# Optimization experiments

Hardware: AMD Instinct MI355X
Metric: run time of the kernel (lower is better)

Reference implementation:

```python
import jax, jax.numpy as jnp
import numpy as np

ETYPES = ((0, 2), (4, 6))  # per-metapath edge-type indices into the doubled r_vec table
ALPHA = 3.0


def celu3(x):
    return jax.nn.celu(x, alpha=ALPHA)


def cmul(a, b):
    # complex multiply, last dim = (real, imag)
    re = a[..., 0] * b[..., 0] - a[..., 1] * b[..., 1]
    im = a[..., 0] * b[..., 1] + a[..., 1] * b[..., 0]
    return jnp.stack([re, im], axis=-1)


def setup_inputs() -> dict:
    key = jax.random.key(0)
    ks = jax.random.split(key, 10)
    N, H, heads, M, E, P = 50000, 64, 4, 2, 250000, 3
    R, FH = 4, 128
    D = heads * H
    return {
        "features": jax.random.normal(ks[0], (N, H), jnp.float32),
        "r_vec": jax.random.normal(ks[1], (R, H // 2, 2), jnp.float32),
        "attn1_w": jax.random.normal(ks[2], (heads, H), jnp.float32) * 0.1,
        "attn2": jax.random.normal(ks[3], (1, heads, H), jnp.float32) * 0.1,
        "fw1": jax.random.normal(ks[4], (2 * FH, D), jnp.float32) * 0.05,
        "fb1": jnp.zeros((2 * FH,), jnp.float32),
        "fw2": jax.random.normal(ks[5], (FH, 2 * FH), jnp.float32) * 0.05,
        "fb2": jnp.zeros((FH,), jnp.float32),
        "fw3": jax.random.normal(ks[6], (1, FH), jnp.float32) * 0.05,
        "instances": jax.random.randint(ks[7], (M, E, P), 0, N, jnp.int32),
    }


def reference(features, r_vec, attn1_w, attn2, fw1, fb1, fw2, fb2, fw3, instances):
    N, H = features.shape
    M, E, P = instances.shape
    heads = attn1_w.shape[0]
    # unit-modulus rotations + conjugates: [2R, H/2, 2], even=r, odd=conj(r)
    rv = r_vec / jnp.linalg.norm(r_vec, axis=2, keepdims=True)
    conj = rv * jnp.array([1.0, -1.0], rv.dtype)
    rv2 = jnp.stack([rv, conj], axis=1).reshape(-1, H // 2, 2)

    per_path = []
    for m in range(M):
        inst = instances[m]  # [E, P]
        # backward cumulative rotation: final_r[i] = prod_{j>=i} r_{etype[j]}, final_r[P-1]=1
        ident = jnp.stack([jnp.ones(H // 2, rv.dtype), jnp.zeros(H // 2, rv.dtype)], axis=-1)
        frs = [ident]
        for i in range(P - 2, -1, -1):
            frs.insert(0, cmul(frs[0], rv2[ETYPES[m][i]]))
        fr = jnp.stack(frs)  # [P, H/2, 2]
        # gather features along metapath and rotate (last position rotated by identity)
        edata = features[inst].reshape(E, P, H // 2, 2)
        rot = cmul(edata, fr[None])
        me = jnp.mean(rot.reshape(E, P, H), axis=1)  # [E, H]
        se = celu3(me) * jax.nn.sigmoid(me)  # gated metapath embedding
        eft = celu3(se)  # same across heads in original (tiled)
        seg = inst[:, 0]  # target node per instance
        a1 = celu3(features[seg] @ attn1_w.T)  # [E, heads]
        a2 = jnp.einsum('eh,kh->ek', eft, attn2[0])  # [E, heads]
        a = celu3(a1 + a2)
        # segment softmax over each node's instance set
        amax = jax.ops.segment_max(a, seg, num_segments=N)
        ex = jnp.exp(a - amax[seg])
        den = jax.ops.segment_sum(ex, seg, num_segments=N)
        attn = ex / den[seg]  # [E, heads]
        hsum = jax.ops.segment_sum(attn[:, :, None] * eft[:, None, :], seg, num_segments=N)
        per_path.append(celu3(hsum).reshape(N, heads * H))  # empty nodes -> 0

    z = jnp.stack(per_path, axis=1)  # [N, M, D]
    t = celu3(z @ fw1.T + fb1)
    t = celu3(t @ fw2.T + fb2)
    w = (t @ fw3.T).mean(axis=0)  # [M, 1]
    beta = jax.nn.softmax(w, axis=0)
    out = (beta * z).sum(axis=1)  # [N, D]
    return out
```

## Files before the change

kernel.cpp:

```cpp
#include <hip/hip_runtime.h>
#include <hip/hip_bf16.h>

typedef unsigned short u16;
typedef unsigned int   u32;
typedef short bf16x8 __attribute__((ext_vector_type(8)));
typedef float f32x4  __attribute__((ext_vector_type(4)));

#define CAP 64

__device__ inline float b2f(u16 u){ return __builtin_bit_cast(float, (u32)u << 16); }
__device__ inline u16 f2b(float f){
  u32 x = __builtin_bit_cast(u32, f);
  x += 0x7fffu + ((x >> 16) & 1u);
  return (u16)(x >> 16);
}
__device__ inline u32 pk2(float lo, float hi){
  float2 f; f.x = lo; f.y = hi;
  __hip_bfloat162 h = __float22bfloat162_rn(f);
  u32 r; __builtin_memcpy(&r, &h, 4);
  return r;
}
__device__ inline void up2(u32 u, float& lo, float& hi){
  lo = __builtin_bit_cast(float, u << 16);
  hi = __builtin_bit_cast(float, u & 0xffff0000u);
}
__device__ inline float fexp(float x){ return __expf(x); }
__device__ inline float celu3(float x){
  return x > 0.f ? x : 3.f * (__expf(x * (1.f/3.f)) - 1.f);
}
__device__ inline float sigm(float x){ return 1.f / (1.f + __expf(-x)); }

__global__ __launch_bounds__(256) void conv_kernel(
    const float* __restrict__ src, u16* __restrict__ dst, int n8)
{
  int i = blockIdx.x * 256 + threadIdx.x;
  if (i >= n8) return;
  float4 a = ((const float4*)src)[2*i], b = ((const float4*)src)[2*i + 1];
  uint4 o;
  o.x = pk2(a.x, a.y);
  o.y = pk2(a.z, a.w);
  o.z = pk2(b.x, b.y);
  o.w = pk2(b.z, b.w);
  ((uint4*)dst)[i] = o;
}

__global__ __launch_bounds__(256) void a1_kernel(
    const float* __restrict__ feat, const float* __restrict__ attn1,
    u16* __restrict__ featb, float* __restrict__ a1c, int N)
{
  __shared__ float w1s[256];
  int t = threadIdx.x;
  w1s[t] = attn1[t];
  __syncthreads();
  int g = t >> 4, l = t & 15;
  int n = blockIdx.x * 16 + g;
  if (n >= N) return;
  float4 x = ((const float4*)feat)[(size_t)n*16 + l];
  uint2 o;
  o.x = pk2(x.x, x.y);
  o.y = pk2(x.z, x.w);
  ((uint2*)featb)[(size_t)n*16 + l] = o;
  float d[4];
  #pragma unroll
  for (int k = 0; k < 4; ++k){
    int wb = k*64 + l*4;
    d[k] = x.x*w1s[wb] + x.y*w1s[wb+1] + x.z*w1s[wb+2] + x.w*w1s[wb+3];
  }
  #pragma unroll
  for (int off = 8; off; off >>= 1){
    #pragma unroll
    for (int k = 0; k < 4; ++k) d[k] += __shfl_xor(d[k], off);
  }
  if (l == 0){
    float4 av;
    av.x = celu3(d[0]); av.y = celu3(d[1]);
    av.z = celu3(d[2]); av.w = celu3(d[3]);
    ((float4*)a1c)[n] = av;
  }
}

__global__ void fr_kernel(const float* __restrict__ rvec, float* __restrict__ fr){
  int c = threadIdx.x;
  if (c >= 32) return;
  for (int m = 0; m < 2; ++m){
    float ar = rvec[(2*m)*64 + c*2],   ai = rvec[(2*m)*64 + c*2 + 1];
    float br = rvec[(2*m+1)*64 + c*2], bi = rvec[(2*m+1)*64 + c*2 + 1];
    float na = rsqrtf(ar*ar + ai*ai); ar *= na; ai *= na;
    float nb = rsqrtf(br*br + bi*bi); br *= nb; bi *= nb;
    float* f = fr + m*128;
    f[c*2]        = br*ar - bi*ai;
    f[c*2 + 1]    = br*ai + bi*ar;
    f[64 + c*2]   = br;
    f[64 + c*2+1] = bi;
  }
}

__global__ __launch_bounds__(256) void edge_kernel(
    const u16* __restrict__ featb, const int* __restrict__ inst,
    const float* __restrict__ fr, const float* __restrict__ a1c,
    const float* __restrict__ attn2, u16* __restrict__ eft,
    float* __restrict__ a_ws, int* __restrict__ cnt, int* __restrict__ bucket,
    int E, int N)
{
  __shared__ float frs[128];
  __shared__ float w2s[256];
  int m = blockIdx.y;
  int t = threadIdx.x;
  if (t < 128) frs[t] = fr[m*128 + t];
  w2s[t] = attn2[t];
  __syncthreads();

  int g = t >> 4, l = t & 15;
  int e = blockIdx.x * 16 + g;
  if (e >= E) return;
  int base = (m*E + e)*3;
  int i0 = inst[base], i1 = inst[base+1], i2 = inst[base+2];

  const uint2* fb = (const uint2*)featb;
  uint2 v0 = fb[(size_t)i0*16 + l];
  uint2 v1 = fb[(size_t)i1*16 + l];
  uint2 v2 = fb[(size_t)i2*16 + l];
  float f0[4], f1[4], f2v[4];
  up2(v0.x, f0[0], f0[1]); up2(v0.y, f0[2], f0[3]);
  up2(v1.x, f1[0], f1[1]); up2(v1.y, f1[2], f1[3]);
  up2(v2.x, f2v[0], f2v[1]); up2(v2.y, f2v[2], f2v[3]);

  float4 R0 = *(const float4*)&frs[4*l];
  float4 R1 = *(const float4*)&frs[64 + 4*l];

  float mre0 = (f0[0]*R0.x - f0[1]*R0.y + f1[0]*R1.x - f1[1]*R1.y + f2v[0]) * (1.f/3.f);
  float mim0 = (f0[0]*R0.y + f0[1]*R0.x + f1[0]*R1.y + f1[1]*R1.x + f2v[1]) * (1.f/3.f);
  float mre1 = (f0[2]*R0.z - f0[3]*R0.w + f1[2]*R1.z - f1[3]*R1.w + f2v[2]) * (1.f/3.f);
  float mim1 = (f0[2]*R0.w + f0[3]*R0.z + f1[2]*R1.w + f1[3]*R1.z + f2v[3]) * (1.f/3.f);

  float ef[4], s;
  s = celu3(mre0) * sigm(mre0); ef[0] = celu3(s);
  s = celu3(mim0) * sigm(mim0); ef[1] = celu3(s);
  s = celu3(mre1) * sigm(mre1); ef[2] = celu3(s);
  s = celu3(mim1) * sigm(mim1); ef[3] = celu3(s);

  uint2 uo;
  uo.x = pk2(ef[0], ef[1]);
  uo.y = pk2(ef[2], ef[3]);
  ((uint2*)eft)[(size_t)(m*E + e)*16 + l] = uo;

  float d2[4];
  #pragma unroll
  for (int k = 0; k < 4; ++k){
    int wb = k*64 + l*4;
    d2[k] = ef[0]*w2s[wb] + ef[1]*w2s[wb+1] + ef[2]*w2s[wb+2] + ef[3]*w2s[wb+3];
  }
  #pragma unroll
  for (int off = 8; off; off >>= 1){
    #pragma unroll
    for (int k = 0; k < 4; ++k) d2[k] += __shfl_xor(d2[k], off);
  }
  if (l == 0){
    float4 a1v = ((const float4*)a1c)[i0];
    float4 av;
    av.x = celu3(a1v.x + d2[0]);
    av.y = celu3(a1v.y + d2[1]);
    av.z = celu3(a1v.z + d2[2]);
    av.w = celu3(a1v.w + d2[3]);
    ((float4*)a_ws)[m*E + e] = av;
    int pos = atomicAdd(&cnt[m*N + i0], 1);
    if (pos < CAP) bucket[(size_t)(m*N + i0)*CAP + pos] = e;
  }
}

__global__ __launch_bounds__(256) void seg_kernel(
    const float* __restrict__ a_ws, const u16* __restrict__ eft,
    const int* __restrict__ cnt, const int* __restrict__ bucket,
    u16* __restrict__ z, int E, int N)
{
  int m = blockIdx.y;
  int n = blockIdx.x * 4 + (threadIdx.x >> 6);
  if (n >= N) return;
  int lane = threadIdx.x & 63;
  int sidx = m*N + n;
  int deg = cnt[sidx]; if (deg > CAP) deg = CAP;

  float h0=0.f, h1=0.f, h2=0.f, h3=0.f;
  float d0=0.f, d1=0.f, d2=0.f, d3=0.f;
  if (deg > 0){
    const int* bk = bucket + (size_t)sidx * CAP;
    size_t ebase = (size_t)m * E;

    int e = (lane < deg) ? bk[lane] : 0;
    float w0 = 0.f, w1 = 0.f, w2 = 0.f, w3 = 0.f;
    if (lane < deg){
      float4 av = ((const float4*)a_ws)[ebase + e];
      w0 = fexp(av.x); w1 = fexp(av.y); w2 = fexp(av.z); w3 = fexp(av.w);
    }

    const u16* ep = eft + ebase*64;
    for (int j = 0; j < deg; ++j){
      int   ej  = __shfl(e,  j);
      float a0j = __shfl(w0, j), a1j = __shfl(w1, j);
      float a2j = __shfl(w2, j), a3j = __shfl(w3, j);
      float ev = b2f(ep[(size_t)ej*64 + lane]);
      h0 += a0j*ev; h1 += a1j*ev; h2 += a2j*ev; h3 += a3j*ev;
      d0 += a0j;    d1 += a1j;    d2 += a2j;    d3 += a3j;
    }
    h0 /= d0; h1 /= d1; h2 /= d2; h3 /= d3;
  }
  u16* zr = z + (size_t)sidx*256 + lane;
  zr[0]   = f2b(celu3(h0));
  zr[64]  = f2b(celu3(h1));
  zr[128] = f2b(celu3(h2));
  zr[192] = f2b(celu3(h3));
}

__global__ __launch_bounds__(256, 6) void mlp_kernel(
    const u16* __restrict__ z, const u16* __restrict__ fw1b, const float* __restrict__ fb1,
    const u16* __restrict__ fw2b, const float* __restrict__ fb2, const float* __restrict__ fw3,
    float* __restrict__ waccP, int rows, int N)
{
  __shared__ u16 buf[32][264];
  __shared__ float fw3s[128];
  __shared__ float sPart[4][32];
  int tid = threadIdx.x;
  int row0 = blockIdx.x * 32;

  if (tid < 128) fw3s[tid] = fw3[tid];

  const uint4* zg = (const uint4*)z;
  #pragma unroll
  for (int it = 0; it < 4; ++it){
    int idx = it*256 + tid;
    int row = idx >> 5;
    int c8  = idx & 31;
    uint4 v = make_uint4(0u,0u,0u,0u);
    int gr = row0 + row;
    if (gr < rows) v = zg[(size_t)gr*32 + c8];
    *(uint4*)&buf[row][c8*8] = v;
  }
  __syncthreads();

  int wv = tid >> 6, lane = tid & 63, lr = lane & 15, quad = lane >> 4;
  f32x4 zero4 = {0.f, 0.f, 0.f, 0.f};

  f32x4 acc[2][4];
  #pragma unroll
  for (int a = 0; a < 2; ++a)
    #pragma unroll
    for (int b = 0; b < 4; ++b) acc[a][b] = zero4;

  const u16* wb1 = fw1b + (size_t)(wv*64 + lr)*256 + quad*8;
  #pragma unroll
  for (int ks = 0; ks < 8; ++ks){
    bf16x8 bfr[4];
    #pragma unroll
    for (int nt = 0; nt < 4; ++nt)
      bfr[nt] = *(const bf16x8*)(wb1 + nt*16*256 + ks*32);
    #pragma unroll
    for (int mt = 0; mt < 2; ++mt){
      bf16x8 af = *(const bf16x8*)&buf[mt*16 + lr][ks*32 + quad*8];
      #pragma unroll
      for (int nt = 0; nt < 4; ++nt)
        acc[mt][nt] = __builtin_amdgcn_mfma_f32_16x16x32_bf16(af, bfr[nt], acc[mt][nt], 0, 0, 0);
    }
  }
  __syncthreads();
  #pragma unroll
  for (int nt = 0; nt < 4; ++nt){
    int col = wv*64 + nt*16 + lr;
    float bias = fb1[col];
    #pragma unroll
    for (int mt = 0; mt < 2; ++mt)
      #pragma unroll
      for (int ri = 0; ri < 4; ++ri){
        int row = mt*16 + quad*4 + ri;
        buf[row][col] = f2b(celu3(acc[mt][nt][ri] + bias));
      }
  }
  __syncthreads();

  f32x4 acc2[2][2];
  #pragma unroll
  for (int a = 0; a < 2; ++a){ acc2[a][0] = zero4; acc2[a][1] = zero4; }
  const u16* wb2 = fw2b + (size_t)(wv*32 + lr)*256 + quad*8;
  #pragma unroll
  for (int ks = 0; ks < 8; ++ks){
    bf16x8 cfr[2];
    cfr[0] = *(const bf16x8*)(wb2 + ks*32);
    cfr[1] = *(const bf16x8*)(wb2 + 16*256 + ks*32);
    #pragma unroll
    for (int mt = 0; mt < 2; ++mt){
      bf16x8 af = *(const bf16x8*)&buf[mt*16 + lr][ks*32 + quad*8];
      acc2[mt][0] = __builtin_amdgcn_mfma_f32_16x16x32_bf16(af, cfr[0], acc2[mt][0], 0, 0, 0);
      acc2[mt][1] = __builtin_amdgcn_mfma_f32_16x16x32_bf16(af, cfr[1], acc2[mt][1], 0, 0, 0);
    }
  }

  float ps[2][4];
  #pragma unroll
  for (int mt = 0; mt < 2; ++mt)
    #pragma unroll
    for (int ri = 0; ri < 4; ++ri) ps[mt][ri] = 0.f;
  #pragma unroll
  for (int nt = 0; nt < 2; ++nt){
    int col = wv*32 + nt*16 + lr;
    float bias = fb2[col];
    float w3 = fw3s[col];
    #pragma unroll
    for (int mt = 0; mt < 2; ++mt)
      #pragma unroll
      for (int ri = 0; ri < 4; ++ri)
        ps[mt][ri] += celu3(acc2[mt][nt][ri] + bias) * w3;
  }
  #pragma unroll
  for (int off = 8; off; off >>= 1)
    #pragma unroll
    for (int mt = 0; mt < 2; ++mt)
      #pragma unroll
      for (int ri = 0; ri < 4; ++ri)
        ps[mt][ri] += __shfl_xor(ps[mt][ri], off);
  if (lr == 0){
    #pragma unroll
    for (int mt = 0; mt < 2; ++mt)
      #pragma unroll
      for (int ri = 0; ri < 4; ++ri)
        sPart[wv][mt*16 + quad*4 + ri] = ps[mt][ri];
  }
  __syncthreads();

  if (tid < 32){
    float s = sPart[0][tid] + sPart[1][tid] + sPart[2][tid] + sPart[3][tid];
    int gr = row0 + tid;
    if (gr >= rows) s = 0.f;
    float s0 = (gr < N) ? s : 0.f;
    float s1 = (gr < N) ? 0.f : s;
    #pragma unroll
    for (int off = 16; off; off >>= 1){
      s0 += __shfl_xor(s0, off);
      s1 += __shfl_xor(s1, off);
    }
    if (tid == 0){
      int slot = blockIdx.x & 63;
      atomicAdd(&waccP[slot],      s0);
      atomicAdd(&waccP[64 + slot], s1);
    }
  }
}

__global__ void beta_kernel(float* __restrict__ wacc, float invN){
  int t = threadIdx.x;
  float s0 = wacc[t], s1 = wacc[64 + t];
  #pragma unroll
  for (int off = 32; off; off >>= 1){
    s0 += __shfl_xor(s0, off);
    s1 += __shfl_xor(s1, off);
  }
  if (t == 0){
    float w0 = s0*invN, w1 = s1*invN;
    float mx = fmaxf(w0, w1);
    float e0 = __expf(w0 - mx), e1 = __expf(w1 - mx);
    float s = e0 + e1;
    wacc[128] = e0 / s;
    wacc[129] = e1 / s;
  }
}

__global__ __launch_bounds__(256) void out_kernel(
    const u16* __restrict__ z, const float* __restrict__ wacc,
    float* __restrict__ out, int total)
{
  int idx = blockIdx.x * 256 + threadIdx.x;
  if (idx*8 >= total) return;
  float b0 = wacc[128], b1 = wacc[129];
  uint4 u0 = ((const uint4*)z)[idx];
  uint4 u1 = ((const uint4*)z)[(total >> 3) + idx];
  float a0,a1v,c0,c1;
  float4 o;
  up2(u0.x, a0, a1v); up2(u1.x, c0, c1);
  o.x = b0*a0 + b1*c0; o.y = b0*a1v + b1*c1;
  up2(u0.y, a0, a1v); up2(u1.y, c0, c1);
  o.z = b0*a0 + b1*c0; o.w = b0*a1v + b1*c1;
  ((float4*)out)[idx*2] = o;
  up2(u0.z, a0, a1v); up2(u1.z, c0, c1);
  o.x = b0*a0 + b1*c0; o.y = b0*a1v + b1*c1;
  up2(u0.w, a0, a1v); up2(u1.w, c0, c1);
  o.z = b0*a0 + b1*c0; o.w = b0*a1v + b1*c1;
  ((float4*)out)[idx*2 + 1] = o;
}

extern "C" void kernel_launch(void* const* d_in, const int* in_sizes, int n_in,
                              void* d_out, int out_size, void* d_ws, size_t ws_size,
                              hipStream_t stream)
{
  (void)n_in; (void)out_size; (void)ws_size;
  const float* feat  = (const float*)d_in[0];
  const float* rvec  = (const float*)d_in[1];
  const float* attn1 = (const float*)d_in[2];
  const float* attn2 = (const float*)d_in[3];
  const float* fw1   = (const float*)d_in[4];
  const float* fb1   = (const float*)d_in[5];
  const float* fw2   = (const float*)d_in[6];
  const float* fb2   = (const float*)d_in[7];
  const float* fw3   = (const float*)d_in[8];
  const int*   inst  = (const int*)d_in[9];

  int N = in_sizes[0] / 64;
  int E = in_sizes[9] / 6;

  char* ws = (char*)d_ws;
  u16*   z      = (u16*)ws;                            size_t zB = (size_t)2*N*256*2;
  u16*   eft    = (u16*)(ws + zB);                     size_t eB = (size_t)2*E*64*2;
  float* a_ws   = (float*)(ws + zB + eB);              size_t aB = (size_t)2*E*4*4;
  int*   bucket = (int*)(ws + zB + eB + aB);           size_t bB = (size_t)2*N*CAP*4;
  int*   cnt    = (int*)(ws + zB + eB + aB + bB);      size_t cB = (size_t)2*N*4;
  u16*   featb  = (u16*)(ws + zB + eB + aB + bB + cB); size_t fB = (size_t)N*64*2;
  float* a1c    = (float*)(ws + zB + eB + aB + bB + cB + fB);  size_t a1B = (size_t)N*4*4;
  u16*   fw1b   = (u16*)(ws + zB + eB + aB + bB + cB + fB + a1B);
  u16*   fw2b   = fw1b + 256*256;
  float* fr     = (float*)(fw2b + 128*256);
  float* wacc   = fr + 256;

  hipMemsetAsync(cnt, 0, cB, stream);
  hipMemsetAsync(wacc, 0, 128*sizeof(float), stream);

  a1_kernel<<<(N + 15)/16, 256, 0, stream>>>(feat, attn1, featb, a1c, N);
  conv_kernel<<<(256*256/8 + 255)/256, 256, 0, stream>>>(fw1, fw1b, 256*256/8);
  conv_kernel<<<(128*256/8 + 255)/256, 256, 0, stream>>>(fw2, fw2b, 128*256/8);
  fr_kernel<<<1, 64, 0, stream>>>(rvec, fr);
  edge_kernel<<<dim3((E + 15)/16, 2), 256, 0, stream>>>(
      featb, inst, fr, a1c, attn2, eft, a_ws, cnt, bucket, E, N);
  seg_kernel<<<dim3((N + 3)/4, 2), 256, 0, stream>>>(a_ws, eft, cnt, bucket, z, E, N);
  mlp_kernel<<<(2*N + 31)/32, 256, 0, stream>>>(z, fw1b, fb1, fw2b, fb2, fw3, wacc, 2*N, N);
  beta_kernel<<<1, 64, 0, stream>>>(wacc, 1.f/(float)N);
  out_kernel<<<((N*256/8) + 255)/256, 256, 0, stream>>>(z, wacc, (float*)d_out, N*256);
}
```

Before: 310.2 us.

## Retile MLP kernel to 64 rows, 8 waves with register-resident weight fragments

The MLP kernel now processes 64 rows per block with 512 threads (8 waves), each wave owning a narrower column slice (32 cols in layer 1, 16 in layer 2). All weight fragments for the wave are preloaded into registers up front, and the z tile load is issued to registers before the LDS store, so global loads overlap. This halves per-row weight traffic and moves layer-2 weight loads ahead of the barrier. The cost is higher register pressure and fewer, larger blocks.

```diff
diff --git a/kernel.cpp b/kernel.cpp
--- a/kernel.cpp
+++ b/kernel.cpp
@@ -211,63 +211,75 @@
   zr[192] = f2b(celu3(h3));
 }
 
-__global__ __launch_bounds__(256, 6) void mlp_kernel(
+__global__ __launch_bounds__(512, 4) void mlp_kernel(
     const u16* __restrict__ z, const u16* __restrict__ fw1b, const float* __restrict__ fb1,
     const u16* __restrict__ fw2b, const float* __restrict__ fb2, const float* __restrict__ fw3,
     float* __restrict__ waccP, int rows, int N)
 {
-  __shared__ u16 buf[32][264];
+  __shared__ u16 buf[64][264];
   __shared__ float fw3s[128];
-  __shared__ float sPart[4][32];
+  __shared__ float sPart[8][64];
   int tid = threadIdx.x;
-  int row0 = blockIdx.x * 32;
+  int row0 = blockIdx.x * 64;
+  int wv = tid >> 6, lane = tid & 63, lr = lane & 15, quad = lane >> 4;
+
+  const uint4* zg = (const uint4*)z;
+  uint4 zr4[4];
+  #pragma unroll
+  for (int it = 0; it < 4; ++it){
+    int idx = it*512 + tid;
+    int row = idx >> 5, c8 = idx & 31;
+    int gr = row0 + row;
+    zr4[it] = make_uint4(0u,0u,0u,0u);
+    if (gr < rows) zr4[it] = zg[(size_t)gr*32 + c8];
+  }
+
+  const u16* wb1 = fw1b + (size_t)(wv*32 + lr)*256 + quad*8;
+  bf16x8 B1[2][8];
+  #pragma unroll
+  for (int nt = 0; nt < 2; ++nt)
+    #pragma unroll
+    for (int ks = 0; ks < 8; ++ks)
+      B1[nt][ks] = *(const bf16x8*)(wb1 + nt*16*256 + ks*32);
 
   if (tid < 128) fw3s[tid] = fw3[tid];
 
-  const uint4* zg = (const uint4*)z;
   #pragma unroll
   for (int it = 0; it < 4; ++it){
-    int idx = it*256 + tid;
-    int row = idx >> 5;
-    int c8  = idx & 31;
-    uint4 v = make_uint4(0u,0u,0u,0u);
-    int gr = row0 + row;
-    if (gr < rows) v = zg[(size_t)gr*32 + c8];
-    *(uint4*)&buf[row][c8*8] = v;
-  }
-  __syncthreads();
-
-  int wv = tid >> 6, lane = tid & 63, lr = lane & 15, quad = lane >> 4;
+    int idx = it*512 + tid;
+    int row = idx >> 5, c8 = idx & 31;
+    *(uint4*)&buf[row][c8*8] = zr4[it];
+  }
+  __syncthreads();
+
   f32x4 zero4 = {0.f, 0.f, 0.f, 0.f};
 
-  f32x4 acc[2][4];
-  #pragma unroll
-  for (int a = 0; a < 2; ++a)
-    #pragma unroll
-    for (int b = 0; b < 4; ++b) acc[a][b] = zero4;
-
-  const u16* wb1 = fw1b + (size_t)(wv*64 + lr)*256 + quad*8;
+  f32x4 acc[4][2];
+  #pragma unroll
+  for (int a = 0; a < 4; ++a){ acc[a][0] = zero4; acc[a][1] = zero4; }
   #pragma unroll
   for (int ks = 0; ks < 8; ++ks){
-    bf16x8 bfr[4];
-    #pragma unroll
-    for (int nt = 0; nt < 4; ++nt)
-      bfr[nt] = *(const bf16x8*)(wb1 + nt*16*256 + ks*32);
-    #pragma unroll
-    for (int mt = 0; mt < 2; ++mt){
+    #pragma unroll
+    for (int mt = 0; mt < 4; ++mt){
       bf16x8 af = *(const bf16x8*)&buf[mt*16 + lr][ks*32 + quad*8];
-      #pragma unroll
-      for (int nt = 0; nt < 4; ++nt)
-        acc[mt][nt] = __builtin_amdgcn_mfma_f32_16x16x32_bf16(af, bfr[nt], acc[mt][nt], 0, 0, 0);
-    }
-  }
-  __syncthreads();
-  #pragma unroll
-  for (int nt = 0; nt < 4; ++nt){
-    int col = wv*64 + nt*16 + lr;
+      acc[mt][0] = __builtin_amdgcn_mfma_f32_16x16x32_bf16(af, B1[0][ks], acc[mt][0], 0, 0, 0);
+      acc[mt][1] = __builtin_amdgcn_mfma_f32_16x16x32_bf16(af, B1[1][ks], acc[mt][1], 0, 0, 0);
+    }
+  }
+
+  const u16* wb2 = fw2b + (size_t)(wv*16 + lr)*256 + quad*8;
+  bf16x8 B2[8];
+  #pragma unroll
+  for (int ks = 0; ks < 8; ++ks)
+    B2[ks] = *(const bf16x8*)(wb2 + ks*32);
+
+  __syncthreads();
+  #pragma unroll
+  for (int nt = 0; nt < 2; ++nt){
+    int col = wv*32 + nt*16 + lr;
     float bias = fb1[col];
     #pragma unroll
-    for (int mt = 0; mt < 2; ++mt)
+    for (int mt = 0; mt < 4; ++mt)
       #pragma unroll
       for (int ri = 0; ri < 4; ++ri){
         int row = mt*16 + quad*4 + ri;
@@ -276,63 +288,55 @@
   }
   __syncthreads();
 
-  f32x4 acc2[2][2];
-  #pragma unroll
-  for (int a = 0; a < 2; ++a){ acc2[a][0] = zero4; acc2[a][1] = zero4; }
-  const u16* wb2 = fw2b + (size_t)(wv*32 + lr)*256 + quad*8;
+  f32x4 acc2[4];
+  #pragma unroll
+  for (int a = 0; a < 4; ++a) acc2[a] = zero4;
   #pragma unroll
   for (int ks = 0; ks < 8; ++ks){
-    bf16x8 cfr[2];
-    cfr[0] = *(const bf16x8*)(wb2 + ks*32);
-    cfr[1] = *(const bf16x8*)(wb2 + 16*256 + ks*32);
-    #pragma unroll
-    for (int mt = 0; mt < 2; ++mt){
+    #pragma unroll
+    for (int mt = 0; mt < 4; ++mt){
       bf16x8 af = *(const bf16x8*)&buf[mt*16 + lr][ks*32 + quad*8];
-      acc2[mt][0] = __builtin_amdgcn_mfma_f32_16x16x32_bf16(af, cfr[0], acc2[mt][0], 0, 0, 0);
-      acc2[mt][1] = __builtin_amdgcn_mfma_f32_16x16x32_bf16(af, cfr[1], acc2[mt][1], 0, 0, 0);
-    }
-  }
-
-  float ps[2][4];
-  #pragma unroll
-  for (int mt = 0; mt < 2; ++mt)
-    #pragma unroll
-    for (int ri = 0; ri < 4; ++ri) ps[mt][ri] = 0.f;
-  #pragma unroll
-  for (int nt = 0; nt < 2; ++nt){
-    int col = wv*32 + nt*16 + lr;
-    float bias = fb2[col];
+      acc2[mt] = __builtin_amdgcn_mfma_f32_16x16x32_bf16(af, B2[ks], acc2[mt], 0, 0, 0);
+    }
+  }
+
+  {
+    int col = wv*16 + lr;
+    float bias2 = fb2[col];
     float w3 = fw3s[col];
-    #pragma unroll
-    for (int mt = 0; mt < 2; ++mt)
+    float ps[4][4];
+    #pragma unroll
+    for (int mt = 0; mt < 4; ++mt)
       #pragma unroll
       for (int ri = 0; ri < 4; ++ri)
-        ps[mt][ri] += celu3(acc2[mt][nt][ri] + bias) * w3;
-  }
-  #pragma unroll
-  for (int off = 8; off; off >>= 1)
-    #pragma unroll
-    for (int mt = 0; mt < 2; ++mt)
+        ps[mt][ri] = celu3(acc2[mt][ri] + bias2) * w3;
+    #pragma unroll
+    for (int off = 8; off; off >>= 1)
       #pragma unroll
-      for (int ri = 0; ri < 4; ++ri)
-        ps[mt][ri] += __shfl_xor(ps[mt][ri], off);
-  if (lr == 0){
-    #pragma unroll
-    for (int mt = 0; mt < 2; ++mt)
+      for (int mt = 0; mt < 4; ++mt)
+        #pragma unroll
+        for (int ri = 0; ri < 4; ++ri)
+          ps[mt][ri] += __shfl_xor(ps[mt][ri], off);
+    if (lr == 0){
       #pragma unroll
-      for (int ri = 0; ri < 4; ++ri)
-        sPart[wv][mt*16 + quad*4 + ri] = ps[mt][ri];
-  }
-  __syncthreads();
-
-  if (tid < 32){
-    float s = sPart[0][tid] + sPart[1][tid] + sPart[2][tid] + sPart[3][tid];
+      for (int mt = 0; mt < 4; ++mt)
+        #pragma unroll
+        for (int ri = 0; ri < 4; ++ri)
+          sPart[wv][mt*16 + quad*4 + ri] = ps[mt][ri];
+    }
+  }
+  __syncthreads();
+
+  if (tid < 64){
+    float s = 0.f;
+    #pragma unroll
+    for (int w = 0; w < 8; ++w) s += sPart[w][tid];
     int gr = row0 + tid;
     if (gr >= rows) s = 0.f;
     float s0 = (gr < N) ? s : 0.f;
     float s1 = (gr < N) ? 0.f : s;
     #pragma unroll
-    for (int off = 16; off; off >>= 1){
+    for (int off = 32; off; off >>= 1){
       s0 += __shfl_xor(s0, off);
       s1 += __shfl_xor(s1, off);
     }
@@ -427,7 +431,7 @@
   edge_kernel<<<dim3((E + 15)/16, 2), 256, 0, stream>>>(
       featb, inst, fr, a1c, attn2, eft, a_ws, cnt, bucket, E, N);
   seg_kernel<<<dim3((N + 3)/4, 2), 256, 0, stream>>>(a_ws, eft, cnt, bucket, z, E, N);
-  mlp_kernel<<<(2*N + 31)/32, 256, 0, stream>>>(z, fw1b, fb1, fw2b, fb2, fw3, wacc, 2*N, N);
+  mlp_kernel<<<(2*N + 63)/64, 512, 0, stream>>>(z, fw1b, fb1, fw2b, fb2, fw3, wacc, 2*N, N);
   beta_kernel<<<1, 64, 0, stream>>>(wacc, 1.f/(float)N);
   out_kernel<<<((N*256/8) + 255)/256, 256, 0, stream>>>(z, wacc, (float*)d_out, N*256);
 }
```

Result: faster. 285.9 us (-7.8%).
